# Optimization experiments

Measured on AMD Instinct MI355X. Metric: run time of the kernel, lower is better.

Reference implementation:

```python
import jax, jax.numpy as jnp
import numpy as np

MAX_RANGE = 100.0


def _conv3x3(x, w, b):
    # x: [B,C,H,W], w: [2,C,3,3], b: [2]
    y = jax.lax.conv_general_dilated(
        x, w, window_strides=(1, 1), padding='SAME',
        dimension_numbers=('NCHW', 'OIHW', 'NCHW'))
    return y + b[None, :, None, None]


def setup_inputs() -> dict:
    key = jax.random.key(0)
    k1, k2, k3 = jax.random.split(key, 3)
    B, C, H, W = 4, 64, 64, 64
    x = jax.random.normal(k1, (B, C, H, W), dtype=jnp.float32)
    conv_w = jax.random.normal(k2, (2, C, 3, 3), dtype=jnp.float32) * 0.05
    conv_b = jax.random.normal(k3, (2,), dtype=jnp.float32) * 0.05
    return {'x': x, 'conv_w': conv_w, 'conv_b': conv_b}


def reference(x, conv_w, conv_b):
    # alpha, beta: [B,1,H,W]
    ab = MAX_RANGE * jnp.tanh(_conv3x3(x, conv_w, conv_b))
    alpha, beta = ab[:, 0:1], ab[:, 1:2]

    # Pairwise differences d[b,i,j,h,w] = beta[b]*x[b,i] - x[b,j]  -> [B,C,C,H,W]
    d = beta[:, :, None] * x[:, :, None] - x[:, None, :]
    a = alpha[:, :, None]  # [B,1,1,H,W]

    # softAbs: softmax over the pair {d, -d} weighted by clamped alpha*d logits
    v1 = jnp.clip(d * a, -MAX_RANGE, MAX_RANGE)
    v2 = jnp.clip(-d * a, -MAX_RANGE, MAX_RANGE)
    m = jnp.maximum(v1, v2)
    e1 = jnp.exp(v1 - m)
    e2 = jnp.exp(v2 - m)
    p1 = e1 / (e1 + e2)
    sabs = d * (2.0 * p1 - 1.0)  # d*p1 + (-d)*(1-p1)

    # mean over i (the expand dim) -> [B,C,H,W]
    tmp = jnp.mean(sabs, axis=1)

    # softArgMin over channel dim
    sam = jax.nn.softmax(jnp.clip(-tmp * alpha, -MAX_RANGE, MAX_RANGE), axis=1)

    # soft median, keepdims -> [B,1,H,W]
    return jnp.sum(x * sam, axis=1, keepdims=True)
```

## Files before the change

kernel.cpp:

```cpp
#include <hip/hip_runtime.h>
#include <math.h>

#define MAXR 100.0f
#define LOG2E 1.4426950408889634f

__device__ __forceinline__ float exp2_fast(float x) { return __builtin_amdgcn_exp2f(x); }
__device__ __forceinline__ float rcp_fast(float x)  { return __builtin_amdgcn_rcpf(x); }
__device__ __forceinline__ float bcast_lane(float v, int i) {
    return __int_as_float(__builtin_amdgcn_readlane(__float_as_int(v), i));
}

__device__ __forceinline__ float tanh_fast(float s) {
    float E = exp2_fast(2.0f * LOG2E * fabsf(s));
    float t = fmaf(-2.0f, rcp_fast(E + 1.0f), 1.0f);
    return copysignf(t, s);
}

template<int CTRL>
__device__ __forceinline__ float dpp0(float v) {
    return __int_as_float(__builtin_amdgcn_update_dpp(0, __float_as_int(v), CTRL, 0xf, 0xf, true));
}
template<int CTRL>
__device__ __forceinline__ float dppk(float v) {
    return __int_as_float(__builtin_amdgcn_update_dpp(__float_as_int(v), __float_as_int(v), CTRL, 0xf, 0xf, false));
}
__device__ __forceinline__ float wave_sum(float v) {
    v += dpp0<0x111>(v);
    v += dpp0<0x112>(v);
    v += dpp0<0x114>(v);
    v += dpp0<0x118>(v);
    v += dpp0<0x142>(v);
    v += dpp0<0x143>(v);
    return bcast_lane(v, 63);
}
__device__ __forceinline__ float wave_max(float v) {
    v = fmaxf(v, dppk<0x111>(v));
    v = fmaxf(v, dppk<0x112>(v));
    v = fmaxf(v, dppk<0x114>(v));
    v = fmaxf(v, dppk<0x118>(v));
    v = fmaxf(v, dppk<0x142>(v));
    v = fmaxf(v, dppk<0x143>(v));
    return bcast_lane(v, 63);
}

__global__ __launch_bounds__(256) void dsf_fused(const float* __restrict__ x,
                                                 const float* __restrict__ wg,
                                                 const float* __restrict__ bias,
                                                 float* __restrict__ out) {
    __shared__ float xs[64 * 19];

    const int tid  = threadIdx.x;
    const int lane = tid & 63;
    const int wave = tid >> 6;

    const int p0 = blockIdx.x * 4;
    const int b  = p0 >> 12;
    const int h  = (p0 >> 6) & 63;
    const int w0 = p0 & 63;

    float wr0[9], wr1[9];
    #pragma unroll
    for (int k = 0; k < 9; ++k) {
        wr0[k] = wg[lane * 9 + k];
        wr1[k] = wg[576 + lane * 9 + k];
    }
    const float b0 = bias[0], b1 = bias[1];

    const float* xbase = x + b * 262144;
    for (int e = tid; e < 1152; e += 256) {
        int c   = e / 18;
        int rem = e - c * 18;
        int r   = rem / 6;
        int wt  = rem - r * 6;
        int hh  = h + r - 1;
        int ww  = w0 - 1 + wt;
        float v = 0.f;
        if (hh >= 0 && hh < 64 && (unsigned)ww < 64u)
            v = xbase[c * 4096 + hh * 64 + ww];
        xs[c * 19 + rem] = v;
    }
    __syncthreads();

    const float* xc = xs + lane * 19;
    float a0 = 0.f, a1 = 0.f;
    #pragma unroll
    for (int r = 0; r < 3; ++r) {
        #pragma unroll
        for (int t = 0; t < 3; ++t) {
            float xv = xc[r * 6 + wave + t];
            a0 = fmaf(xv, wr0[r * 3 + t], a0);
            a1 = fmaf(xv, wr1[r * 3 + t], a1);
        }
    }
    a0 = wave_sum(a0);
    a1 = wave_sum(a1);
    const float al = MAXR * tanh_fast(a0 + b0);
    const float be = MAXR * tanh_fast(a1 + b1);
    const float aa = fabsf(al);
    const float c2 = 2.0f * LOG2E * aa;

    const float xj = xc[6 + wave + 1];

    float A0 = 0.f, A1 = 0.f, A2 = 0.f, A3 = 0.f;
    #pragma unroll
    for (int i = 0; i < 64; i += 4) {
        float s0 = bcast_lane(xj, i + 0);
        float s1 = bcast_lane(xj, i + 1);
        float s2 = bcast_lane(xj, i + 2);
        float s3 = bcast_lane(xj, i + 3);
        float d0 = fabsf(fmaf(be, s0, -xj));
        float d1 = fabsf(fmaf(be, s1, -xj));
        float d2 = fabsf(fmaf(be, s2, -xj));
        float d3 = fabsf(fmaf(be, s3, -xj));
        float m0 = c2 * d0;
        float m1 = c2 * d1;
        float m2 = c2 * d2;
        float m3 = c2 * d3;
        float mn = fminf(fminf(m0, m1), fminf(m2, m3));
        if (__all(mn >= 28.0f)) {
            A0 += d0; A1 += d1; A2 += d2; A3 += d3;
        } else {
            float E0 = exp2_fast(m0);
            float E1 = exp2_fast(m1);
            float E2 = exp2_fast(m2);
            float E3 = exp2_fast(m3);
            float r0 = rcp_fast(E0 + 1.f);
            float r1 = rcp_fast(E1 + 1.f);
            float r2 = rcp_fast(E2 + 1.f);
            float r3 = rcp_fast(E3 + 1.f);
            A0 = fmaf(d0, fmaf(-2.f, r0, 1.f), A0);
            A1 = fmaf(d1, fmaf(-2.f, r1, 1.f), A1);
            A2 = fmaf(d2, fmaf(-2.f, r2, 1.f), A2);
            A3 = fmaf(d3, fmaf(-2.f, r3, 1.f), A3);
        }
    }
    float A = (A0 + A1) + (A2 + A3);

    float gl = fmaxf(-A * aa * (1.0f / 64.0f), -MAXR);

    float gm = wave_max(gl);
    float ew  = exp2_fast((gl - gm) * LOG2E);
    float den = wave_sum(ew);
    float num = wave_sum(xj * ew);
    if (lane == 0) out[p0 + wave] = num * rcp_fast(den);
}

extern "C" void kernel_launch(void* const* d_in, const int* in_sizes, int n_in,
                              void* d_out, int out_size, void* d_ws, size_t ws_size,
                              hipStream_t stream) {
    const float* x      = (const float*)d_in[0];
    const float* conv_w = (const float*)d_in[1];
    const float* conv_b = (const float*)d_in[2];
    float* out = (float*)d_out;
    (void)d_ws; (void)ws_size;

    dsf_fused<<<4096, 256, 0, stream>>>(x, conv_w, conv_b, out);
}
```

Baseline: 77.78 us.

## Classify saturated softAbs pairs per source lane and sum them in closed form

The pairwise softAbs loop is replaced by a per-source-lane test. Using the wave max and min of x, each lane i is checked for whether beta*x_i lies far enough above or below every x_j that the tanh term saturates for all j. Those lanes are folded in algebraically through wave sums and ballot popcounts. Only the remaining non-saturated lanes go through a wave-uniform scalar loop that evaluates exp/rcp. This removes most per-pair transcendental work when beta is large, but pixels with small |beta| now run a serial loop with no ILP, and the saturation threshold moves from 28 to 29.

Result: faster. 73.51 us (-5.5%).

```diff
diff --git a/kernel.cpp b/kernel.cpp
--- a/kernel.cpp
+++ b/kernel.cpp
@@ -40,6 +40,15 @@
     v = fmaxf(v, dppk<0x118>(v));
     v = fmaxf(v, dppk<0x142>(v));
     v = fmaxf(v, dppk<0x143>(v));
+    return bcast_lane(v, 63);
+}
+__device__ __forceinline__ float wave_min(float v) {
+    v = fminf(v, dppk<0x111>(v));
+    v = fminf(v, dppk<0x112>(v));
+    v = fminf(v, dppk<0x114>(v));
+    v = fminf(v, dppk<0x118>(v));
+    v = fminf(v, dppk<0x142>(v));
+    v = fminf(v, dppk<0x143>(v));
     return bcast_lane(v, 63);
 }
 
@@ -101,40 +110,34 @@
 
     const float xj = xc[6 + wave + 1];
 
-    float A0 = 0.f, A1 = 0.f, A2 = 0.f, A3 = 0.f;
-    #pragma unroll
-    for (int i = 0; i < 64; i += 4) {
-        float s0 = bcast_lane(xj, i + 0);
-        float s1 = bcast_lane(xj, i + 1);
-        float s2 = bcast_lane(xj, i + 2);
-        float s3 = bcast_lane(xj, i + 3);
-        float d0 = fabsf(fmaf(be, s0, -xj));
-        float d1 = fabsf(fmaf(be, s1, -xj));
-        float d2 = fabsf(fmaf(be, s2, -xj));
-        float d3 = fabsf(fmaf(be, s3, -xj));
-        float m0 = c2 * d0;
-        float m1 = c2 * d1;
-        float m2 = c2 * d2;
-        float m3 = c2 * d3;
-        float mn = fminf(fminf(m0, m1), fminf(m2, m3));
-        if (__all(mn >= 28.0f)) {
-            A0 += d0; A1 += d1; A2 += d2; A3 += d3;
-        } else {
-            float E0 = exp2_fast(m0);
-            float E1 = exp2_fast(m1);
-            float E2 = exp2_fast(m2);
-            float E3 = exp2_fast(m3);
-            float r0 = rcp_fast(E0 + 1.f);
-            float r1 = rcp_fast(E1 + 1.f);
-            float r2 = rcp_fast(E2 + 1.f);
-            float r3 = rcp_fast(E3 + 1.f);
-            A0 = fmaf(d0, fmaf(-2.f, r0, 1.f), A0);
-            A1 = fmaf(d1, fmaf(-2.f, r1, 1.f), A1);
-            A2 = fmaf(d2, fmaf(-2.f, r2, 1.f), A2);
-            A3 = fmaf(d3, fmaf(-2.f, r3, 1.f), A3);
-        }
+    const float M  = wave_max(xj);
+    const float mN = wave_min(xj);
+    const float thr = 29.0f * rcp_fast(c2);
+    const float bx  = be * xj;
+
+    const bool isp = bx >= M + thr;
+    const bool isn = bx <= mN - thr;
+    unsigned long long pm = __ballot(isp);
+    unsigned long long nm = __ballot(isn);
+    unsigned long long hm = ~(pm | nm);
+
+    float SP = wave_sum(isp ? bx : 0.0f);
+    float SN = wave_sum(isn ? bx : 0.0f);
+    int   CP = __popcll(pm);
+    int   CN = __popcll(nm);
+
+    float A = (SP - SN) + (float)(CN - CP) * xj;
+
+    while (hm) {
+        int i = __ffsll((long long)hm) - 1;
+        hm &= hm - 1;
+        float s = bcast_lane(xj, i);
+        float d = fabsf(fmaf(be, s, -xj));
+        float m = c2 * d;
+        float E = exp2_fast(m);
+        float r = rcp_fast(E + 1.0f);
+        A = fmaf(d, fmaf(-2.0f, r, 1.0f), A);
     }
-    float A = (A0 + A1) + (A2 + A3);
 
     float gl = fmaxf(-A * aa * (1.0f / 64.0f), -MAXR);
 
```
